# Kernel tuning notes

Hardware: AMD Instinct MI355X
Metric: run time of the kernel (lower is better)

The kernel has to match this reference:

```python
import jax, jax.numpy as jnp
import numpy as np

B, T, F = 32, 512, 4096
H = 128            # num_lstm
NUM_CLASSES = 2    # dense outputs = NUM_CLASSES + 1 (CTC blank)


def setup_inputs() -> dict:
    key = jax.random.key(0)
    ks = jax.random.split(key, 6)
    x = jax.random.normal(ks[0], (B, T, F), dtype=jnp.float32)
    # Keras LSTM params: kernel [F, 4H], recurrent_kernel [H, 4H], bias [4H]
    # (gate order i, f, c, o). Glorot-ish scaling for stability.
    Wk = jax.random.normal(ks[1], (F, 4 * H), dtype=jnp.float32) / np.sqrt(F)
    Wr = jax.random.normal(ks[2], (H, 4 * H), dtype=jnp.float32) / np.sqrt(H)
    b = jnp.zeros((4 * H,), dtype=jnp.float32).at[H:2 * H].set(1.0)  # unit_forget_bias
    Wd = jax.random.normal(ks[3], (H, NUM_CLASSES + 1), dtype=jnp.float32) / np.sqrt(H)
    bd = jnp.zeros((NUM_CLASSES + 1,), dtype=jnp.float32)
    return {"x": x, "Wk": Wk, "Wr": Wr, "b": b, "Wd": Wd, "bd": bd}


def _lstm(x, Wk, Wr, b):
    # Precompute input projections for all timesteps (big GEMM once).
    z = jnp.einsum("btf,fg->btg", x, Wk) + b          # [B, T, 4H]
    z = jnp.transpose(z, (1, 0, 2))                    # [T, B, 4H]

    def step(carry, z_t):
        h, c = carry
        g = z_t + h @ Wr                               # [B, 4H]
        i = jax.nn.sigmoid(g[:, 0 * H:1 * H])
        f = jax.nn.sigmoid(g[:, 1 * H:2 * H])
        cc = jnp.tanh(g[:, 2 * H:3 * H])
        o = jax.nn.sigmoid(g[:, 3 * H:4 * H])
        c = f * c + i * cc
        h = o * jnp.tanh(c)
        return (h, c), h

    h0 = jnp.zeros((x.shape[0], H), dtype=x.dtype)
    c0 = jnp.zeros((x.shape[0], H), dtype=x.dtype)
    _, hs = jax.lax.scan(step, (h0, c0), z)            # hs: [T, B, H]
    return jnp.transpose(hs, (1, 0, 2))                # [B, T, H]


def reference(x, Wk, Wr, b, Wd, bd):
    # Inference-mode forward (dropout/recurrent_dropout inactive).
    h = _lstm(x, Wk, Wr, b)                            # [B, T, H]
    return h @ Wd + bd                                 # [B, T, num_classes+1]
```

## Files before the change

### kernel.cpp

```cpp
#include <hip/hip_runtime.h>
#include <hip/hip_bf16.h>
#include <hip/hip_fp16.h>
#include <math.h>

#define B_  32
#define T_  512
#define F_  4096
#define H_  128
#define G4H 512
#define NCLS 3
#define M_  (B_ * T_)
#define KSTEPS 128

typedef _Float16 f16x8 __attribute__((ext_vector_type(8)));
typedef _Float16 f16x4 __attribute__((ext_vector_type(4)));
typedef float    f32x4 __attribute__((ext_vector_type(4)));

__global__ __launch_bounds__(256) void cvt_wkT(
    const float* __restrict__ Wk, _Float16* __restrict__ btK)
{
    __shared__ float ls[64][65];
    const int k0 = blockIdx.x * 64;
    const int n0 = blockIdx.y * 64;
    const int tid = threadIdx.x;

    {
        int r  = tid >> 4;
        int c4 = (tid & 15) * 4;
        #pragma unroll
        for (int p = 0; p < 4; ++p) {
            float4 v = *reinterpret_cast<const float4*>(
                &Wk[(size_t)(k0 + r + p * 16) * G4H + n0 + c4]);
            ls[r + p * 16][c4 + 0] = v.x;
            ls[r + p * 16][c4 + 1] = v.y;
            ls[r + p * 16][c4 + 2] = v.z;
            ls[r + p * 16][c4 + 3] = v.w;
        }
    }
    __syncthreads();
    {
        int rn = tid >> 2;
        int ck = (tid & 3) * 16;
        f16x8 h0, h1;
        #pragma unroll
        for (int j = 0; j < 8; ++j) {
            h0[j] = (_Float16)ls[ck + j][rn];
            h1[j] = (_Float16)ls[ck + 8 + j][rn];
        }
        const int n    = n0 + rn;
        const int kg   = k0 + ck;
        const int kblk = kg >> 5;
        const int kk   = kg & 31;
        const int g0   = kk >> 3;
        const int sw   = (n >> 1) & 3;
        _Float16* base = btK + (size_t)kblk * (512 * 32) + (size_t)n * 32;
        *reinterpret_cast<f16x8*>(base + ((g0 ^ sw) << 3))       = h0;
        *reinterpret_cast<f16x8*>(base + (((g0 + 1) ^ sw) << 3)) = h1;
    }
}

__global__ __launch_bounds__(256) void cvt_wrT(
    const float* __restrict__ Wr, _Float16* __restrict__ wrT)
{
    __shared__ float ls[64][65];
    const int k0 = blockIdx.x * 64;
    const int n0 = blockIdx.y * 64;
    const int tid = threadIdx.x;
    {
        int r  = tid >> 4;
        int c4 = (tid & 15) * 4;
        #pragma unroll
        for (int p = 0; p < 4; ++p) {
            float4 v = *reinterpret_cast<const float4*>(
                &Wr[(size_t)(k0 + r + p * 16) * G4H + n0 + c4]);
            ls[r + p * 16][c4 + 0] = v.x;
            ls[r + p * 16][c4 + 1] = v.y;
            ls[r + p * 16][c4 + 2] = v.z;
            ls[r + p * 16][c4 + 3] = v.w;
        }
    }
    __syncthreads();
    {
        int rn = tid >> 2;
        int ck = (tid & 3) * 16;
        f16x8 h0, h1;
        #pragma unroll
        for (int j = 0; j < 8; ++j) {
            h0[j] = (_Float16)ls[ck + j][rn];
            h1[j] = (_Float16)ls[ck + 8 + j][rn];
        }
        _Float16* dst = &wrT[(size_t)(n0 + rn) * H_ + k0 + ck];
        *reinterpret_cast<f16x8*>(dst)     = h0;
        *reinterpret_cast<f16x8*>(dst + 8) = h1;
    }
}

__device__ __forceinline__ void lds_barrier() {
    asm volatile("s_waitcnt lgkmcnt(0)" ::: "memory");
    __builtin_amdgcn_s_barrier();
    asm volatile("" ::: "memory");
}

__global__ __launch_bounds__(512, 4) void gemm_fused(
    const float* __restrict__ x, const _Float16* __restrict__ btK,
    const float* __restrict__ bias, float* __restrict__ z)
{
    __shared__ __align__(16) _Float16 As[2][64 * 32];

    const int tid = threadIdx.x;
    const int w   = tid >> 6;
    const int l   = tid & 63;
    const int fr  = l & 15;
    const int q   = l >> 4;

    const int bid   = blockIdx.x;
    const int xcd   = bid & 7;
    const int idx   = bid >> 3;
    const int mt    = xcd * 32 + (idx >> 1);
    const int ntile = idx & 1;
    const int m0    = mt * 64;
    const int n0    = ntile * 256;

    const int ar = tid >> 3;
    const int hc = (tid & 7) * 4;
    const int abyte = ((((hc >> 3) ^ ((ar >> 1) & 3)) << 4) | ((hc << 1) & 15));
    const float* xrow = x + (size_t)(m0 + ar) * F_ + hc;

    const int nA = n0 + w * 32 + fr;
    const int nB = nA + 16;
    const _Float16* bp0 = btK + (size_t)nA * 32 + ((q ^ ((nA >> 1) & 3)) << 3);
    const _Float16* bp1 = btK + (size_t)nB * 32 + ((q ^ ((nB >> 1) & 3)) << 3);

    #define LOADB(t, bfv)                                                     \
    {                                                                         \
        bfv[0] = *reinterpret_cast<const f16x8*>(bp0 + (size_t)(t) * 16384);  \
        bfv[1] = *reinterpret_cast<const f16x8*>(bp1 + (size_t)(t) * 16384);  \
    }

    #define LOADX(t) (*reinterpret_cast<const float4*>(xrow + (size_t)(t) * 32))

    #define WRITE_A(v, buf)                                                   \
    {                                                                         \
        f16x4 hh; hh[0] = (_Float16)v.x; hh[1] = (_Float16)v.y;               \
        hh[2] = (_Float16)v.z; hh[3] = (_Float16)v.w;                         \
        *reinterpret_cast<f16x4*>(                                            \
            reinterpret_cast<char*>(&As[buf][0]) + ar * 64 + abyte) = hh;     \
    }

    #define COMPUTE(buf, bfv)                                                 \
    {                                                                         \
        f16x8 af[4];                                                          \
        _Pragma("unroll")                                                     \
        for (int i = 0; i < 4; ++i) {                                         \
            int r   = i * 16 + fr;                                            \
            int off = r * 64 + ((q ^ ((r >> 1) & 3)) << 4);                   \
            af[i] = *reinterpret_cast<const f16x8*>(                          \
                reinterpret_cast<const char*>(&As[buf][0]) + off);            \
        }                                                                     \
        _Pragma("unroll")                                                     \
        for (int i = 0; i < 4; ++i)                                           \
            _Pragma("unroll")                                                 \
            for (int j = 0; j < 2; ++j)                                       \
                acc[i][j] = __builtin_amdgcn_mfma_f32_16x16x32_f16(           \
                    af[i], bfv[j], acc[i][j], 0, 0, 0);                       \
    }

    f32x4 acc[4][2] = {};
    f16x8 bfA[2], bfB[2];
    float4 xa, xb;

    xa = LOADX(0); xb = LOADX(1);
    LOADB(0, bfA) LOADB(1, bfB)
    WRITE_A(xa, 0)
    lds_barrier();

    for (int t = 0; t < 126; t += 2) {
        xa = LOADX(t + 2);
        WRITE_A(xb, 1)
        COMPUTE(0, bfA)
        LOADB(t + 2, bfA)
        lds_barrier();
        xb = LOADX(t + 3);
        WRITE_A(xa, 0)
        COMPUTE(1, bfB)
        LOADB(t + 3, bfB)
        lds_barrier();
    }
    WRITE_A(xb, 1)
    COMPUTE(0, bfA)
    lds_barrier();
    COMPUTE(1, bfB)

    #undef LOADB
    #undef LOADX
    #undef WRITE_A
    #undef COMPUTE

    #pragma unroll
    for (int j = 0; j < 2; ++j) {
        const int nn = n0 + w * 32 + j * 16 + fr;
        const int ch = (nn & 127) * 4 + (nn >> 7);
        const float bj = bias[nn];
        #pragma unroll
        for (int i = 0; i < 4; ++i)
            #pragma unroll
            for (int r = 0; r < 4; ++r)
                z[(size_t)(m0 + i * 16 + q * 4 + r) * G4H + ch]
                    = acc[i][j][r] + bj;
    }
}

__device__ __forceinline__ float sig_f(float x) {
    return __builtin_amdgcn_rcpf(
        1.0f + __builtin_amdgcn_exp2f(-1.442695040888963f * x));
}
__device__ __forceinline__ float tanh_f(float x) {
    return 1.0f - 2.0f * __builtin_amdgcn_rcpf(
        1.0f + __builtin_amdgcn_exp2f(2.885390081777927f * x));
}

__global__ __launch_bounds__(512, 2) void lstm_mfma(
    const float* __restrict__ z,
    const _Float16* __restrict__ wrT,
    float* __restrict__ hs)
{
    const int b    = blockIdx.x;
    const int tid  = threadIdx.x;
    const int w    = tid >> 6;
    const int lane = tid & 63;
    const int l15  = lane & 15;
    const int q    = lane >> 4;
    const int jj   = w * 16 + l15;

    __shared__ __align__(16) _Float16 hA[2][128];

    f16x8 bf[4][4];
    #pragma unroll
    for (int g = 0; g < 4; ++g)
        #pragma unroll
        for (int kf = 0; kf < 4; ++kf)
            bf[g][kf] = *reinterpret_cast<const f16x8*>(
                &wrT[(size_t)(g * H_ + jj) * H_ + kf * 32 + q * 8]);

    float cstate = 0.f;
    if (tid < 128) reinterpret_cast<unsigned int*>(hA)[tid] = 0u;

    const float* zrow  = z  + (size_t)b * T_ * G4H + jj * 4;
    float*       hbase = hs + (size_t)b * T_ * H_;

    const f32x4 zero4 = {0.f, 0.f, 0.f, 0.f};

    float4 zP0 = *reinterpret_cast<const float4*>(zrow + (size_t)(0 << 9));
    float4 zP1 = *reinterpret_cast<const float4*>(zrow + (size_t)(1 << 9));
    float4 zP2 = *reinterpret_cast<const float4*>(zrow + (size_t)(2 << 9));
    float4 zP3 = *reinterpret_cast<const float4*>(zrow + (size_t)(3 << 9));

    __syncthreads();

    #define LSTM_STEP(t, CUR, ZZ)                                             \
    {                                                                         \
        f16x8 af0 = *reinterpret_cast<const f16x8*>(&hA[CUR][0 * 32 + q * 8]);\
        f16x8 af1 = *reinterpret_cast<const f16x8*>(&hA[CUR][1 * 32 + q * 8]);\
        f16x8 af2 = *reinterpret_cast<const f16x8*>(&hA[CUR][2 * 32 + q * 8]);\
        f16x8 af3 = *reinterpret_cast<const f16x8*>(&hA[CUR][3 * 32 + q * 8]);\
        float zt0_ = ZZ.x, zt1_ = ZZ.y, zt2_ = ZZ.z, zt3_ = ZZ.w;             \
        ZZ = *reinterpret_cast<const float4*>(                                \
            zrow + (size_t)((((t) + 4) & (T_ - 1)) << 9));                    \
        float gv[4];                                                          \
        _Pragma("unroll")                                                     \
        for (int g = 0; g < 4; ++g) {                                         \
            f32x4 aA = __builtin_amdgcn_mfma_f32_16x16x32_f16(                \
                af0, bf[g][0], zero4, 0, 0, 0);                               \
            aA = __builtin_amdgcn_mfma_f32_16x16x32_f16(                      \
                af1, bf[g][1], aA, 0, 0, 0);                                  \
            f32x4 aB = __builtin_amdgcn_mfma_f32_16x16x32_f16(                \
                af2, bf[g][2], zero4, 0, 0, 0);                               \
            aB = __builtin_amdgcn_mfma_f32_16x16x32_f16(                      \
                af3, bf[g][3], aB, 0, 0, 0);                                  \
            gv[g] = aA[0] + aB[0];                                           \
        }                                                                     \
        float iv = sig_f(gv[0] + zt0_);                                       \
        float fv = sig_f(gv[1] + zt1_);                                       \
        float cc = tanh_f(gv[2] + zt2_);                                      \
        float ov = sig_f(gv[3] + zt3_);                                       \
        cstate = fv * cstate + iv * cc;                                       \
        float h = ov * tanh_f(cstate);                                        \
        if (q == 0) {                                                         \
            hA[CUR ^ 1][jj] = (_Float16)h;                                    \
            hbase[((t) << 7) + jj] = h;                                       \
        }                                                                     \
        lds_barrier();                                                        \
    }

    for (int t = 0; t < T_; t += 4) {
        LSTM_STEP(t,     0, zP0)
        LSTM_STEP(t + 1, 1, zP1)
        LSTM_STEP(t + 2, 0, zP2)
        LSTM_STEP(t + 3, 1, zP3)
    }
    #undef LSTM_STEP
}

__global__ __launch_bounds__(256) void dense_out(
    const float* __restrict__ hs, const float* __restrict__ Wd,
    const float* __restrict__ bd, float* __restrict__ out)
{
    int idx = blockIdx.x * 256 + threadIdx.x;
    if (idx >= B_ * T_ * NCLS) return;
    int cls = idx % NCLS;
    int row = idx / NCLS;
    const float* h = hs + (size_t)row * H_;
    float acc = bd[cls];
    #pragma unroll 8
    for (int k = 0; k < H_; ++k) acc += h[k] * Wd[k * NCLS + cls];
    out[idx] = acc;
}

extern "C" void kernel_launch(void* const* d_in, const int* in_sizes, int n_in,
                              void* d_out, int out_size, void* d_ws, size_t ws_size,
                              hipStream_t stream)
{
    const float* x  = (const float*)d_in[0];
    const float* Wk = (const float*)d_in[1];
    const float* Wr = (const float*)d_in[2];
    const float* b  = (const float*)d_in[3];
    const float* Wd = (const float*)d_in[4];
    const float* bd = (const float*)d_in[5];
    float* out = (float*)d_out;

    float*     z   = (float*)d_ws;
    float*     hs  = z + (size_t)M_ * G4H;
    _Float16*  btK = (_Float16*)(hs + (size_t)M_ * H_);
    _Float16*  wrT = btK + (size_t)G4H * F_;

    cvt_wkT<<<dim3(F_ / 64, G4H / 64), 256, 0, stream>>>(Wk, btK);
    cvt_wrT<<<dim3(H_ / 64, G4H / 64), 256, 0, stream>>>(Wr, wrT);
    gemm_fused<<<512, 512, 0, stream>>>(x, btK, b, z);
    lstm_mfma<<<B_, 512, 0, stream>>>(z, wrT, hs);
    int total = B_ * T_ * NCLS;
    dense_out<<<(total + 255) / 256, 256, 0, stream>>>(hs, Wd, bd, out);
}
```

Measured before the change: 375.0 us.

## Retile input GEMM to 128-column tiles and split LSTM scan into two launches

The input-projection GEMM now uses 256-thread blocks with 128-wide N tiles, 1024 blocks in total, and each thread stages two A rows. The z output goes back to the natural gate-major column layout, so the LSTM kernel gathers its four gate values with scalar strided loads. The recurrence is split into two launches of 256 timesteps each, with cell state and fp16 hidden state saved to workspace between them. The aim is more GEMM parallelism and smaller per-block register use, at the cost of reading x from HBM twice as often, less vectorised z loads, and an extra launch plus state round-trip in the serial LSTM.

```diff
diff --git a/kernel.cpp b/kernel.cpp
--- a/kernel.cpp
+++ b/kernel.cpp
@@ -101,7 +101,7 @@
     asm volatile("" ::: "memory");
 }
 
-__global__ __launch_bounds__(512, 4) void gemm_fused(
+__global__ __launch_bounds__(256, 4) void gemm_fused(
     const float* __restrict__ x, const _Float16* __restrict__ btK,
     const float* __restrict__ bias, float* __restrict__ z)
 {
@@ -116,15 +116,16 @@
     const int bid   = blockIdx.x;
     const int xcd   = bid & 7;
     const int idx   = bid >> 3;
-    const int mt    = xcd * 32 + (idx >> 1);
-    const int ntile = idx & 1;
+    const int mt    = xcd * 32 + (idx >> 2);
+    const int ntile = idx & 3;
     const int m0    = mt * 64;
-    const int n0    = ntile * 256;
+    const int n0    = ntile * 128;
 
     const int ar = tid >> 3;
     const int hc = (tid & 7) * 4;
     const int abyte = ((((hc >> 3) ^ ((ar >> 1) & 3)) << 4) | ((hc << 1) & 15));
-    const float* xrow = x + (size_t)(m0 + ar) * F_ + hc;
+    const float* xrow0 = x + (size_t)(m0 + ar) * F_ + hc;
+    const float* xrow1 = xrow0 + (size_t)32 * F_;
 
     const int nA = n0 + w * 32 + fr;
     const int nB = nA + 16;
@@ -137,14 +138,21 @@
         bfv[1] = *reinterpret_cast<const f16x8*>(bp1 + (size_t)(t) * 16384);  \
     }
 
-    #define LOADX(t) (*reinterpret_cast<const float4*>(xrow + (size_t)(t) * 32))
-
-    #define WRITE_A(v, buf)                                                   \
-    {                                                                         \
-        f16x4 hh; hh[0] = (_Float16)v.x; hh[1] = (_Float16)v.y;               \
-        hh[2] = (_Float16)v.z; hh[3] = (_Float16)v.w;                         \
-        *reinterpret_cast<f16x4*>(                                            \
-            reinterpret_cast<char*>(&As[buf][0]) + ar * 64 + abyte) = hh;     \
+    #define LOADX(t, va, vb)                                                  \
+    {                                                                         \
+        va = *reinterpret_cast<const float4*>(xrow0 + (size_t)(t) * 32);      \
+        vb = *reinterpret_cast<const float4*>(xrow1 + (size_t)(t) * 32);      \
+    }
+
+    #define WRITE_A(va, vb, buf)                                              \
+    {                                                                         \
+        f16x4 h0; h0[0] = (_Float16)va.x; h0[1] = (_Float16)va.y;             \
+        h0[2] = (_Float16)va.z; h0[3] = (_Float16)va.w;                       \
+        f16x4 h1; h1[0] = (_Float16)vb.x; h1[1] = (_Float16)vb.y;             \
+        h1[2] = (_Float16)vb.z; h1[3] = (_Float16)vb.w;                       \
+        char* ab = reinterpret_cast<char*>(&As[buf][0]);                      \
+        *reinterpret_cast<f16x4*>(ab + ar * 64 + abyte) = h0;                 \
+        *reinterpret_cast<f16x4*>(ab + (ar + 32) * 64 + abyte) = h1;          \
     }
 
     #define COMPUTE(buf, bfv)                                                 \
@@ -167,26 +175,26 @@
 
     f32x4 acc[4][2] = {};
     f16x8 bfA[2], bfB[2];
-    float4 xa, xb;
-
-    xa = LOADX(0); xb = LOADX(1);
+    float4 xa0, xa1, xb0, xb1;
+
+    LOADX(0, xa0, xa1) LOADX(1, xb0, xb1)
     LOADB(0, bfA) LOADB(1, bfB)
-    WRITE_A(xa, 0)
+    WRITE_A(xa0, xa1, 0)
     lds_barrier();
 
     for (int t = 0; t < 126; t += 2) {
-        xa = LOADX(t + 2);
-        WRITE_A(xb, 1)
+        LOADX(t + 2, xa0, xa1)
+        WRITE_A(xb0, xb1, 1)
         COMPUTE(0, bfA)
         LOADB(t + 2, bfA)
         lds_barrier();
-        xb = LOADX(t + 3);
-        WRITE_A(xa, 0)
+        LOADX(t + 3, xb0, xb1)
+        WRITE_A(xa0, xa1, 0)
         COMPUTE(1, bfB)
         LOADB(t + 3, bfB)
         lds_barrier();
     }
-    WRITE_A(xb, 1)
+    WRITE_A(xb0, xb1, 1)
     COMPUTE(0, bfA)
     lds_barrier();
     COMPUTE(1, bfB)
@@ -199,13 +207,12 @@
     #pragma unroll
     for (int j = 0; j < 2; ++j) {
         const int nn = n0 + w * 32 + j * 16 + fr;
-        const int ch = (nn & 127) * 4 + (nn >> 7);
         const float bj = bias[nn];
         #pragma unroll
         for (int i = 0; i < 4; ++i)
             #pragma unroll
             for (int r = 0; r < 4; ++r)
-                z[(size_t)(m0 + i * 16 + q * 4 + r) * G4H + ch]
+                z[(size_t)(m0 + i * 16 + q * 4 + r) * G4H + nn]
                     = acc[i][j][r] + bj;
     }
 }
@@ -222,7 +229,10 @@
 __global__ __launch_bounds__(512, 2) void lstm_mfma(
     const float* __restrict__ z,
     const _Float16* __restrict__ wrT,
-    float* __restrict__ hs)
+    float* __restrict__ hs,
+    float* __restrict__ cst,
+    _Float16* __restrict__ h16,
+    int t0)
 {
     const int b    = blockIdx.x;
     const int tid  = threadIdx.x;
@@ -242,18 +252,32 @@
             bf[g][kf] = *reinterpret_cast<const f16x8*>(
                 &wrT[(size_t)(g * H_ + jj) * H_ + kf * 32 + q * 8]);
 
-    float cstate = 0.f;
-    if (tid < 128) reinterpret_cast<unsigned int*>(hA)[tid] = 0u;
-
-    const float* zrow  = z  + (size_t)b * T_ * G4H + jj * 4;
+    float cstate;
+    if (t0 == 0) {
+        if (tid < 128) reinterpret_cast<unsigned int*>(hA)[tid] = 0u;
+        cstate = 0.f;
+    } else {
+        if (tid < 64)
+            reinterpret_cast<unsigned int*>(hA[0])[tid] =
+                reinterpret_cast<const unsigned int*>(h16 + (size_t)b * H_)[tid];
+        cstate = cst[(size_t)b * H_ + jj];
+    }
+
+    const float* zq    = z  + (size_t)b * T_ * G4H + jj;
     float*       hbase = hs + (size_t)b * T_ * H_;
 
     const f32x4 zero4 = {0.f, 0.f, 0.f, 0.f};
 
-    float4 zP0 = *reinterpret_cast<const float4*>(zrow + (size_t)(0 << 9));
-    float4 zP1 = *reinterpret_cast<const float4*>(zrow + (size_t)(1 << 9));
-    float4 zP2 = *reinterpret_cast<const float4*>(zrow + (size_t)(2 << 9));
-    float4 zP3 = *reinterpret_cast<const float4*>(zrow + (size_t)(3 << 9));
+    #define LOADZ(t, d)                                                       \
+    {                                                                         \
+        int zo = (((t) & (T_ - 1)) << 9);                                     \
+        d.x = zq[zo];       d.y = zq[zo + 128];                               \
+        d.z = zq[zo + 256]; d.w = zq[zo + 384];                               \
+    }
+
+    float4 zP0, zP1, zP2, zP3;
+    LOADZ(t0 + 0, zP0) LOADZ(t0 + 1, zP1)
+    LOADZ(t0 + 2, zP2) LOADZ(t0 + 3, zP3)
 
     __syncthreads();
 
@@ -264,8 +288,7 @@
         f16x8 af2 = *reinterpret_cast<const f16x8*>(&hA[CUR][2 * 32 + q * 8]);\
         f16x8 af3 = *reinterpret_cast<const f16x8*>(&hA[CUR][3 * 32 + q * 8]);\
         float zt0_ = ZZ.x, zt1_ = ZZ.y, zt2_ = ZZ.z, zt3_ = ZZ.w;             \
-        ZZ = *reinterpret_cast<const float4*>(                                \
-            zrow + (size_t)((((t) + 4) & (T_ - 1)) << 9));                    \
+        LOADZ((t) + 4, ZZ)                                                    \
         float gv[4];                                                          \
         _Pragma("unroll")                                                     \
         for (int g = 0; g < 4; ++g) {                                         \
@@ -277,7 +300,7 @@
                 af2, bf[g][2], zero4, 0, 0, 0);                               \
             aB = __builtin_amdgcn_mfma_f32_16x16x32_f16(                      \
                 af3, bf[g][3], aB, 0, 0, 0);                                  \
-            gv[g] = aA[0] + aB[0];                                           \
+            gv[g] = aA[0] + aB[0];                                            \
         }                                                                     \
         float iv = sig_f(gv[0] + zt0_);                                       \
         float fv = sig_f(gv[1] + zt1_);                                       \
@@ -292,13 +315,19 @@
         lds_barrier();                                                        \
     }
 
-    for (int t = 0; t < T_; t += 4) {
+    for (int t = t0; t < t0 + 256; t += 4) {
         LSTM_STEP(t,     0, zP0)
         LSTM_STEP(t + 1, 1, zP1)
         LSTM_STEP(t + 2, 0, zP2)
         LSTM_STEP(t + 3, 1, zP3)
     }
     #undef LSTM_STEP
+    #undef LOADZ
+
+    if (q == 0) cst[(size_t)b * H_ + jj] = cstate;
+    if (tid < 64)
+        reinterpret_cast<unsigned int*>(h16 + (size_t)b * H_)[tid] =
+            reinterpret_cast<unsigned int*>(hA[0])[tid];
 }
 
 __global__ __launch_bounds__(256) void dense_out(
@@ -332,11 +361,14 @@
     float*     hs  = z + (size_t)M_ * G4H;
     _Float16*  btK = (_Float16*)(hs + (size_t)M_ * H_);
     _Float16*  wrT = btK + (size_t)G4H * F_;
+    float*     cst = (float*)(wrT + (size_t)G4H * H_);
+    _Float16*  h16 = (_Float16*)(cst + (size_t)B_ * H_);
 
     cvt_wkT<<<dim3(F_ / 64, G4H / 64), 256, 0, stream>>>(Wk, btK);
     cvt_wrT<<<dim3(H_ / 64, G4H / 64), 256, 0, stream>>>(Wr, wrT);
-    gemm_fused<<<512, 512, 0, stream>>>(x, btK, b, z);
-    lstm_mfma<<<B_, 512, 0, stream>>>(z, wrT, hs);
+    gemm_fused<<<1024, 256, 0, stream>>>(x, btK, b, z);
+    lstm_mfma<<<B_, 512, 0, stream>>>(z, wrT, hs, cst, h16, 0);
+    lstm_mfma<<<B_, 512, 0, stream>>>(z, wrT, hs, cst, h16, 256);
     int total = B_ * T_ * NCLS;
     dense_out<<<(total + 255) / 256, 256, 0, stream>>>(hs, Wd, bd, out);
 }
```

Result: slower. 434.2 us (+15.8%).
